# Performance work log

Hardware: AMD Instinct MI355X
Metric: run time of the kernel (lower is better)

Reference implementation:

```python
import jax, jax.numpy as jnp
import numpy as np

NR, NL, K, TOPK, C, B = 4096, 16384, 8, 10, 16, 4
W_OCC, W_MDN, W_INT = 0.2, 1.0, 0.1
LOG2PI = float(np.log(2.0 * np.pi))


def setup_inputs() -> dict:
    key = jax.random.key(0)
    ks = jax.random.split(key, 12)
    radar_indices = jnp.concatenate([
        jax.random.randint(ks[0], (NR, 1), 0, B),
        jax.random.randint(ks[1], (NR, 1), 0, 41),
        jax.random.randint(ks[2], (NR, 2), 0, 176),
    ], axis=1).astype(jnp.int32)
    lidar_indices = jnp.concatenate([
        jax.random.randint(ks[3], (NL, 1), 0, B),
        jax.random.randint(ks[4], (NL, 1), 0, 41),
        jax.random.randint(ks[5], (NL, 2), 0, 176),
    ], axis=1).astype(jnp.int32)
    return {
        'mu_off': jax.random.normal(ks[6], (NR, K, 3)) * 2.0,
        'log_sig_off': jax.random.normal(ks[7], (NR, K, 3)) * 0.3,
        'mu_int': jax.random.normal(ks[8], (NR, K, 1)),
        'occ_logit': jax.random.normal(ks[9], (NR, K, 1)),
        'mix_logit': jax.random.normal(ks[10], (NR, K, 1)),
        'lidar_features': jax.random.normal(ks[11], (NL, C)),
        'radar_indices': radar_indices,
        'lidar_indices': lidar_indices,
        'gt_topk': TOPK,
    }


def _match(radar_indices, lidar_indices, topk):
    # per-batch top-k nearest lidar voxels for each radar voxel (vectorized:
    # dense masked distance matrix replaces the per-batch python loop)
    rb, lb = radar_indices[:, 0], lidar_indices[:, 0]
    rpos = radar_indices[:, 1:].astype(jnp.float32)  # (Nr,3) zyx
    lpos = lidar_indices[:, 1:].astype(jnp.float32)  # (Nl,3)
    d2 = ((rpos * rpos).sum(-1)[:, None] + (lpos * lpos).sum(-1)[None, :]
          - 2.0 * (rpos @ lpos.T))  # (Nr,Nl) squared dist, same order as cdist
    same = rb[:, None] == lb[None, :]
    d2 = jnp.where(same, d2, jnp.inf)  # cross-batch pairs excluded
    _, nn_idx = jax.lax.top_k(-d2, topk)  # (Nr,topk) smallest distances
    matched = same.any(axis=1)  # (Nr,)
    offs_zyx = (lidar_indices[nn_idx, 1:]
                - radar_indices[:, None, 1:]).astype(jnp.float32)  # (Nr,topk,3)
    offs_zyx = jnp.where(matched[:, None, None], offs_zyx, 0.0)
    return matched, nn_idx, offs_zyx


def reference(mu_off, log_sig_off, mu_int, occ_logit, mix_logit,
              lidar_features, radar_indices, lidar_indices, gt_topk):
    matched, nn_idx, offs_zyx = _match(radar_indices, lidar_indices, gt_topk)
    gt_feat = jnp.where(matched[:, None, None], lidar_features[nn_idx], 0.0)  # (Nr,T,C)
    y = offs_zyx[..., ::-1]  # flip zyx -> xyz, (Nr,T,3)

    # occupancy BCE-with-logits against matched mask
    occ_any = occ_logit[..., 0].max(axis=1)  # (Nr,)
    tgt = matched.astype(occ_any.dtype)
    occ_loss = (tgt * jax.nn.softplus(-occ_any)
                + (1.0 - tgt) * jax.nn.softplus(occ_any)).mean()

    # MDN log-prob: (Nr,T,K) mixture components
    log_pi = jax.nn.log_softmax(mix_logit[..., 0], axis=1)  # (Nr,K)
    mu_ = mu_off[:, None, :, :]       # (Nr,1,K,3)
    ls_ = log_sig_off[:, None, :, :]
    sigma2 = jnp.exp(2.0 * ls_) + 1e-12
    y_ = y[:, :, None, :]             # (Nr,T,1,3)
    logN = -0.5 * (((y_ - mu_) ** 2) / sigma2 + 2.0 * ls_ + LOG2PI).sum(-1)  # (Nr,T,K)
    log_post = logN + log_pi[:, None, :]
    logp = jax.nn.logsumexp(log_post, axis=-1)  # (Nr,T)

    # masked means emulate boolean-index-then-mean over matched rows
    m = matched.astype(jnp.float32)
    cnt = m.sum()
    T = logp.shape[1]
    mdn_nll = -(logp * m[:, None]).sum() / (cnt * T)

    # intensity loss (C % 4 == 0 path)
    gt_int = gt_feat.reshape(gt_feat.shape[0], gt_feat.shape[1], C // 4, 4)[..., 3].mean(axis=2)  # (Nr,T)
    r = jax.nn.softmax(log_post, axis=-1)  # (Nr,T,K) responsibilities
    term = r * jnp.abs(mu_int[:, None, :, 0] - gt_int[:, :, None])  # (Nr,T,K)
    int_loss = (term * m[:, None, None]).sum() / (cnt * T * r.shape[-1])

    return W_OCC * occ_loss + W_MDN * mdn_nll + W_INT * int_loss
```

## Files before the change

kernel.cpp:

```cpp
#include <hip/hip_runtime.h>
#include <cstdint>

#define NRAD 4096
#define NLID 16384
#define KMIX 8
#define TOPK 10
#define CF   16
#define LOG2PI 1.8378770664093453f

static constexpr unsigned INF_D2 = 62851u;

__device__ __forceinline__ void insert_key(unsigned (&t)[TOPK], unsigned key) {
#pragma unroll
    for (int i = TOPK - 1; i >= 1; --i) {
        unsigned hi = key > t[i - 1] ? key : t[i - 1];
        t[i] = hi < t[i] ? hi : t[i];
    }
    t[0] = key < t[0] ? key : t[0];
}

__device__ __forceinline__ void merge10(unsigned (&t)[TOPK], int lane,
                                        unsigned& mine, unsigned& first, unsigned& tenth) {
#pragma unroll
    for (int r = 0; r < TOPK; ++r) {
        unsigned v = t[0];
#pragma unroll
        for (int off = 32; off >= 1; off >>= 1) {
            unsigned o = __shfl_xor(v, off, 64);
            v = o < v ? o : v;
        }
        if (t[0] == v) {
#pragma unroll
            for (int i = 0; i < TOPK - 1; ++i) t[i] = t[i + 1];
            t[TOPK - 1] = 0xFFFFFFFFu;
        }
        if (lane == r) mine = v;
        if (r == 0) first = v;
        if (r == TOPK - 1) tenth = v;
    }
}

__device__ __forceinline__ float waveReduceSum(float v) {
#pragma unroll
    for (int off = 32; off >= 1; off >>= 1) v += __shfl_down(v, off, 64);
    return v;
}

__global__ __launch_bounds__(1024) void prep_kernel(
        const int* __restrict__ lidar_indices,
        const int* __restrict__ radar_indices,
        unsigned* __restrict__ packed_full,
        uint2* __restrict__ compacted,
        int* __restrict__ rbin,
        int* __restrict__ ctrl) {
    __shared__ int lcur, rcur;
    int tid = threadIdx.x, lane = tid & 63, myb = blockIdx.x;
    if (tid == 0) { lcur = 0; rcur = 0; }
    __syncthreads();

#pragma unroll
    for (int it = 0; it < NLID / 1024; ++it) {
        int i = it * 1024 + tid;
        int4 li = ((const int4*)lidar_indices)[i];
        unsigned pos = ((unsigned)li.y << 16) | ((unsigned)li.z << 8) | (unsigned)li.w;
        bool mine = (li.x == myb);
        if (mine) packed_full[i] = ((unsigned)li.x << 22) | pos;
        unsigned long long mask = __ballot(mine);
        if (mine) {
            int leader = __ffsll(mask) - 1;
            int off = (int)__popcll(mask & ((1ull << lane) - 1ull));
            int s = 0;
            if (lane == leader) s = atomicAdd(&lcur, (int)__popcll(mask));
            s = __shfl(s, leader, 64);
            compacted[myb * NLID + s + off] = make_uint2(pos, (unsigned)i);
        }
    }

#pragma unroll
    for (int it = 0; it < NRAD / 1024; ++it) {
        int r = it * 1024 + tid;
        int rb = radar_indices[r * 4];
        bool mine = (rb == myb);
        unsigned long long mask = __ballot(mine);
        if (mine) {
            int leader = __ffsll(mask) - 1;
            int off = (int)__popcll(mask & ((1ull << lane) - 1ull));
            int s = 0;
            if (lane == leader) s = atomicAdd(&rcur, (int)__popcll(mask));
            s = __shfl(s, leader, 64);
            rbin[myb * NRAD + s + off] = r;
        }
    }

    __syncthreads();
    if (tid == 0) { ctrl[myb] = lcur; ctrl[12 + myb] = rcur; }
    if (myb == 0 && tid >= 64 && tid < 69) ctrl[4 + (tid - 64)] = 0;
}

__global__ __launch_bounds__(256) void topk_kernel(
        const uint2* __restrict__ compacted,
        const unsigned* __restrict__ packed_full,
        const int* __restrict__ ctrl,
        const int* __restrict__ rbin,
        const int* __restrict__ radar_indices,
        int* __restrict__ nn_out, int* __restrict__ matched_out) {
    int lane = threadIdx.x & 63;
    int g = blockIdx.x * 4 + (threadIdx.x >> 6);
    int r0 = ctrl[12], r1 = ctrl[13], r2 = ctrl[14];
    int cum1 = r0, cum2 = r0 + r1, cum3 = cum2 + r2;
    int gb = (g >= cum1) + (g >= cum2) + (g >= cum3);
    int gbase = gb == 0 ? 0 : (gb == 1 ? cum1 : (gb == 2 ? cum2 : cum3));
    int row = rbin[gb * NRAD + (g - gbase)];

    int4 ri = ((const int4*)radar_indices)[row];
    int rb = ri.x, rz = ri.y, ry = ri.z, rx = ri.w;
    int c_cnt = ctrl[rb];

    unsigned t[TOPK];
#pragma unroll
    for (int i = 0; i < TOPK; ++i) t[i] = 0xFFFFFFFFu;

    const uint4* src = (const uint4*)(compacted + rb * NLID);
    int iters = (c_cnt + 127) >> 7;
    uint4 q = src[lane];
    for (int it = 0; it < iters; ++it) {
        uint4 qn = q;
        if (it + 1 < iters) qn = src[(it + 1) * 64 + lane];
        int c0 = (it * 64 + lane) * 2;
        {
            int dz = (int)((q.x >> 16) & 63u)  - rz;
            int dy = (int)((q.x >> 8)  & 255u) - ry;
            int dx = (int)(q.x & 255u)         - rx;
            unsigned d2 = (unsigned)(__mul24(dz, dz) + __mul24(dy, dy) + __mul24(dx, dx));
            unsigned key = (c0 < c_cnt) ? ((d2 << 14) | q.y) : 0xFFFFFFFFu;
            if (key < t[TOPK - 1]) insert_key(t, key);
        }
        {
            int dz = (int)((q.z >> 16) & 63u)  - rz;
            int dy = (int)((q.z >> 8)  & 255u) - ry;
            int dx = (int)(q.z & 255u)         - rx;
            unsigned d2 = (unsigned)(__mul24(dz, dz) + __mul24(dy, dy) + __mul24(dx, dx));
            unsigned key = (c0 + 1 < c_cnt) ? ((d2 << 14) | q.w) : 0xFFFFFFFFu;
            if (key < t[TOPK - 1]) insert_key(t, key);
        }
        q = qn;
    }

    unsigned mine = 0, first = 0, tenth = 0;
    merge10(t, lane, mine, first, tenth);
    bool matched = true;

    if (tenth == 0xFFFFFFFFu) {
#pragma unroll
        for (int i = 0; i < TOPK; ++i) t[i] = 0xFFFFFFFFu;
        for (int it = 0; it < NLID / 256; ++it) {
            uint4 p4 = ((const uint4*)packed_full)[it * 64 + lane];
            unsigned base = it * 256 + lane * 4;
            unsigned ps[4] = {p4.x, p4.y, p4.z, p4.w};
#pragma unroll
            for (int j = 0; j < 4; ++j) {
                unsigned p = ps[j];
                int b  = (int)(p >> 22);
                int dz = (int)((p >> 16) & 63u)  - rz;
                int dy = (int)((p >> 8)  & 255u) - ry;
                int dx = (int)(p & 255u)         - rx;
                unsigned d2 = (unsigned)(__mul24(dz, dz) + __mul24(dy, dy) + __mul24(dx, dx));
                unsigned hi = (b == rb) ? d2 : INF_D2;
                insert_key(t, (hi << 14) | (base + j));
            }
        }
        merge10(t, lane, mine, first, tenth);
        matched = first < (INF_D2 << 14);
    }

    if (lane < TOPK) nn_out[row * TOPK + lane] = (int)(mine & 0x3FFFu);
    if (lane == 0)   matched_out[row] = matched ? 1 : 0;
}

__global__ __launch_bounds__(256) void mdn_kernel(
        const float* __restrict__ mu_off, const float* __restrict__ log_sig_off,
        const float* __restrict__ mu_int, const float* __restrict__ occ_logit,
        const float* __restrict__ mix_logit, const float* __restrict__ lidar_features,
        const int* __restrict__ radar_indices, const int* __restrict__ lidar_indices,
        const int* __restrict__ nn, const int* __restrict__ matched,
        float* __restrict__ accum,
        unsigned* __restrict__ dctr,
        float* __restrict__ out) {
    int gid = blockIdx.x * 256 + threadIdx.x;
    int n  = gid / TOPK;
    int tt = gid - n * TOPK;
    int m  = matched[n];
    float mf = (float)m;
    int nni = nn[gid];

    int4 ri = ((const int4*)radar_indices)[n];
    int4 li = ((const int4*)lidar_indices)[nni];
    float y0 = mf * (float)(li.w - ri.w);
    float y1 = mf * (float)(li.z - ri.z);
    float y2 = mf * (float)(li.y - ri.y);

    float mix[KMIX];
    float mmax = -1e30f;
#pragma unroll
    for (int k = 0; k < KMIX; ++k) {
        mix[k] = mix_logit[n * KMIX + k];
        mmax = fmaxf(mmax, mix[k]);
    }
    float msum = 0.f;
#pragma unroll
    for (int k = 0; k < KMIX; ++k) msum += expf(mix[k] - mmax);
    float logZ = mmax + logf(msum);

    float lpost[KMIX];
    float pmax = -1e30f;
#pragma unroll
    for (int k = 0; k < KMIX; ++k) {
        int bidx = (n * KMIX + k) * 3;
        float mu0 = mu_off[bidx + 0], mu1 = mu_off[bidx + 1], mu2 = mu_off[bidx + 2];
        float l0 = log_sig_off[bidx + 0], l1 = log_sig_off[bidx + 1], l2 = log_sig_off[bidx + 2];
        float s0 = expf(2.f * l0) + 1e-12f;
        float s1 = expf(2.f * l1) + 1e-12f;
        float s2 = expf(2.f * l2) + 1e-12f;
        float d0 = y0 - mu0, d1 = y1 - mu1, d2v = y2 - mu2;
        float q = d0 * d0 / s0 + d1 * d1 / s1 + d2v * d2v / s2
                + 2.f * (l0 + l1 + l2) + 3.f * LOG2PI;
        lpost[k] = -0.5f * q + (mix[k] - logZ);
        pmax = fmaxf(pmax, lpost[k]);
    }
    float ex[KMIX];
    float se = 0.f;
#pragma unroll
    for (int k = 0; k < KMIX; ++k) { ex[k] = expf(lpost[k] - pmax); se += ex[k]; }
    float logp = pmax + logf(se);

    float gt = 0.f;
    if (m) {
        const float* lf = lidar_features + nni * CF;
        gt = 0.25f * (lf[3] + lf[7] + lf[11] + lf[15]);
    }
    float inv_se = 1.f / se;
    float isum = 0.f;
#pragma unroll
    for (int k = 0; k < KMIX; ++k)
        isum += ex[k] * inv_se * fabsf(mu_int[n * KMIX + k] - gt);

    float lp = mf * logp;
    float ip = mf * isum;
    float oc = 0.f, mc = 0.f;
    if (tt == 0) {
        float oa = -1e30f;
#pragma unroll
        for (int k = 0; k < KMIX; ++k) oa = fmaxf(oa, occ_logit[n * KMIX + k]);
        float soft_abs = log1pf(expf(-fabsf(oa)));
        oc = mf * (soft_abs + fmaxf(-oa, 0.f)) + (1.f - mf) * (soft_abs + fmaxf(oa, 0.f));
        mc = mf;
    }

    lp = waveReduceSum(lp); ip = waveReduceSum(ip);
    oc = waveReduceSum(oc); mc = waveReduceSum(mc);
    __shared__ float sA[4], sB[4], sC[4], sD[4];
    int wid = threadIdx.x >> 6, lane = threadIdx.x & 63;
    if (lane == 0) { sA[wid] = lp; sB[wid] = ip; sC[wid] = oc; sD[wid] = mc; }
    __syncthreads();
    if (threadIdx.x == 0) {
        atomicAdd(&accum[0], sA[0] + sA[1] + sA[2] + sA[3]);
        atomicAdd(&accum[1], sB[0] + sB[1] + sB[2] + sB[3]);
        atomicAdd(&accum[2], sC[0] + sC[1] + sC[2] + sC[3]);
        atomicAdd(&accum[3], sD[0] + sD[1] + sD[2] + sD[3]);
        __threadfence();
        unsigned done = atomicAdd(dctr, 1u);
        if (done == gridDim.x - 1) {
            __threadfence();
            float a = __hip_atomic_load(&accum[0], __ATOMIC_RELAXED, __HIP_MEMORY_SCOPE_AGENT);
            float b = __hip_atomic_load(&accum[1], __ATOMIC_RELAXED, __HIP_MEMORY_SCOPE_AGENT);
            float c = __hip_atomic_load(&accum[2], __ATOMIC_RELAXED, __HIP_MEMORY_SCOPE_AGENT);
            float d = __hip_atomic_load(&accum[3], __ATOMIC_RELAXED, __HIP_MEMORY_SCOPE_AGENT);
            float occ_loss = c / (float)NRAD;
            float mdn_nll  = -a / (d * (float)TOPK);
            float int_loss = b / (d * (float)TOPK * (float)KMIX);
            out[0] = 0.2f * occ_loss + mdn_nll + 0.1f * int_loss;
        }
    }
}

extern "C" void kernel_launch(void* const* d_in, const int* in_sizes, int n_in,
                              void* d_out, int out_size, void* d_ws, size_t ws_size,
                              hipStream_t stream) {
    const float* mu_off         = (const float*)d_in[0];
    const float* log_sig_off    = (const float*)d_in[1];
    const float* mu_int         = (const float*)d_in[2];
    const float* occ_logit      = (const float*)d_in[3];
    const float* mix_logit      = (const float*)d_in[4];
    const float* lidar_features = (const float*)d_in[5];
    const int*   radar_indices  = (const int*)d_in[6];
    const int*   lidar_indices  = (const int*)d_in[7];
    float* out = (float*)d_out;

    char* ws = (char*)d_ws;
    unsigned* packed_full = (unsigned*)(ws + 0);
    uint2*    compacted   = (uint2*)(ws + 65536);
    int*      ctrl        = (int*)(ws + 589824);
    int*      nn          = (int*)(ws + 589888);
    int*      matched     = (int*)(ws + 753728);
    int*      rbin        = (int*)(ws + 770112);

    float*    accum = (float*)(ctrl + 4);
    unsigned* dctr  = (unsigned*)(ctrl + 8);

    hipLaunchKernelGGL(prep_kernel, dim3(4), dim3(1024), 0, stream,
                       lidar_indices, radar_indices, packed_full, compacted, rbin, ctrl);
    hipLaunchKernelGGL(topk_kernel, dim3(NRAD / 4), dim3(256), 0, stream,
                       compacted, packed_full, ctrl, rbin, radar_indices, nn, matched);
    hipLaunchKernelGGL(mdn_kernel, dim3(NRAD * TOPK / 256), dim3(256), 0, stream,
                       mu_off, log_sig_off, mu_int, occ_logit, mix_logit,
                       lidar_features, radar_indices, lidar_indices,
                       nn, matched, accum, dctr, out);
}
```

Before: 121.3 us.

## Fuse top-k matching with MDN loss and preload indices in prep kernel

Folds the MDN/intensity/occupancy loss computation into the top-k kernel. Each wave now uses its merged top-k result directly, with lanes below TOPK taking one neighbor each, so the nn/matched global arrays and a third kernel launch go away. The prep kernel also issues all lidar and radar index loads up front into registers so the loads overlap before the ballot/compaction loops. The cost is more register pressure in the fused kernel and only 10 of 64 lanes doing MDN work per wave, and the completion counter now covers 1024 blocks instead of 160.

```diff
diff --git a/kernel.cpp b/kernel.cpp
--- a/kernel.cpp
+++ b/kernel.cpp
@@ -56,15 +56,24 @@
     __shared__ int lcur, rcur;
     int tid = threadIdx.x, lane = tid & 63, myb = blockIdx.x;
     if (tid == 0) { lcur = 0; rcur = 0; }
+
+    int4 li[NLID / 1024];
+#pragma unroll
+    for (int it = 0; it < NLID / 1024; ++it)
+        li[it] = ((const int4*)lidar_indices)[it * 1024 + tid];
+    int rb4[NRAD / 1024];
+#pragma unroll
+    for (int it = 0; it < NRAD / 1024; ++it)
+        rb4[it] = ((const int4*)radar_indices)[it * 1024 + tid].x;
+
     __syncthreads();
 
 #pragma unroll
     for (int it = 0; it < NLID / 1024; ++it) {
         int i = it * 1024 + tid;
-        int4 li = ((const int4*)lidar_indices)[i];
-        unsigned pos = ((unsigned)li.y << 16) | ((unsigned)li.z << 8) | (unsigned)li.w;
-        bool mine = (li.x == myb);
-        if (mine) packed_full[i] = ((unsigned)li.x << 22) | pos;
+        unsigned pos = ((unsigned)li[it].y << 16) | ((unsigned)li[it].z << 8) | (unsigned)li[it].w;
+        bool mine = (li[it].x == myb);
+        if (mine) packed_full[i] = ((unsigned)li[it].x << 22) | pos;
         unsigned long long mask = __ballot(mine);
         if (mine) {
             int leader = __ffsll(mask) - 1;
@@ -79,8 +88,7 @@
 #pragma unroll
     for (int it = 0; it < NRAD / 1024; ++it) {
         int r = it * 1024 + tid;
-        int rb = radar_indices[r * 4];
-        bool mine = (rb == myb);
+        bool mine = (rb4[it] == myb);
         unsigned long long mask = __ballot(mine);
         if (mine) {
             int leader = __ffsll(mask) - 1;
@@ -97,13 +105,19 @@
     if (myb == 0 && tid >= 64 && tid < 69) ctrl[4 + (tid - 64)] = 0;
 }
 
-__global__ __launch_bounds__(256) void topk_kernel(
+__global__ __launch_bounds__(256) void topk_mdn_kernel(
         const uint2* __restrict__ compacted,
         const unsigned* __restrict__ packed_full,
-        const int* __restrict__ ctrl,
+        int* __restrict__ ctrl,
         const int* __restrict__ rbin,
         const int* __restrict__ radar_indices,
-        int* __restrict__ nn_out, int* __restrict__ matched_out) {
+        const int* __restrict__ lidar_indices,
+        const float* __restrict__ mu_off, const float* __restrict__ log_sig_off,
+        const float* __restrict__ mu_int, const float* __restrict__ occ_logit,
+        const float* __restrict__ mix_logit, const float* __restrict__ lidar_features,
+        float* __restrict__ out) {
+    float* accum = (float*)(ctrl + 4);
+    unsigned* dctr = (unsigned*)(ctrl + 8);
     int lane = threadIdx.x & 63;
     int g = blockIdx.x * 4 + (threadIdx.x >> 6);
     int r0 = ctrl[12], r1 = ctrl[13], r2 = ctrl[14];
@@ -173,31 +187,13 @@
         matched = first < (INF_D2 << 14);
     }
 
-    if (lane < TOPK) nn_out[row * TOPK + lane] = (int)(mine & 0x3FFFu);
-    if (lane == 0)   matched_out[row] = matched ? 1 : 0;
-}
-
-__global__ __launch_bounds__(256) void mdn_kernel(
-        const float* __restrict__ mu_off, const float* __restrict__ log_sig_off,
-        const float* __restrict__ mu_int, const float* __restrict__ occ_logit,
-        const float* __restrict__ mix_logit, const float* __restrict__ lidar_features,
-        const int* __restrict__ radar_indices, const int* __restrict__ lidar_indices,
-        const int* __restrict__ nn, const int* __restrict__ matched,
-        float* __restrict__ accum,
-        unsigned* __restrict__ dctr,
-        float* __restrict__ out) {
-    int gid = blockIdx.x * 256 + threadIdx.x;
-    int n  = gid / TOPK;
-    int tt = gid - n * TOPK;
-    int m  = matched[n];
-    float mf = (float)m;
-    int nni = nn[gid];
-
-    int4 ri = ((const int4*)radar_indices)[n];
+    int n = row;
+    float mf = matched ? 1.f : 0.f;
+    int nni = (int)(mine & 0x3FFFu);
     int4 li = ((const int4*)lidar_indices)[nni];
-    float y0 = mf * (float)(li.w - ri.w);
-    float y1 = mf * (float)(li.z - ri.z);
-    float y2 = mf * (float)(li.y - ri.y);
+    float y0 = mf * (float)(li.w - rx);
+    float y1 = mf * (float)(li.z - ry);
+    float y2 = mf * (float)(li.y - rz);
 
     float mix[KMIX];
     float mmax = -1e30f;
@@ -222,9 +218,9 @@
         float s1 = expf(2.f * l1) + 1e-12f;
         float s2 = expf(2.f * l2) + 1e-12f;
         float d0 = y0 - mu0, d1 = y1 - mu1, d2v = y2 - mu2;
-        float q = d0 * d0 / s0 + d1 * d1 / s1 + d2v * d2v / s2
-                + 2.f * (l0 + l1 + l2) + 3.f * LOG2PI;
-        lpost[k] = -0.5f * q + (mix[k] - logZ);
+        float qv = d0 * d0 / s0 + d1 * d1 / s1 + d2v * d2v / s2
+                 + 2.f * (l0 + l1 + l2) + 3.f * LOG2PI;
+        lpost[k] = -0.5f * qv + (mix[k] - logZ);
         pmax = fmaxf(pmax, lpost[k]);
     }
     float ex[KMIX];
@@ -234,7 +230,7 @@
     float logp = pmax + logf(se);
 
     float gt = 0.f;
-    if (m) {
+    if (matched) {
         const float* lf = lidar_features + nni * CF;
         gt = 0.25f * (lf[3] + lf[7] + lf[11] + lf[15]);
     }
@@ -244,10 +240,10 @@
     for (int k = 0; k < KMIX; ++k)
         isum += ex[k] * inv_se * fabsf(mu_int[n * KMIX + k] - gt);
 
-    float lp = mf * logp;
-    float ip = mf * isum;
+    float lp = (lane < TOPK) ? mf * logp : 0.f;
+    float ip = (lane < TOPK) ? mf * isum : 0.f;
     float oc = 0.f, mc = 0.f;
-    if (tt == 0) {
+    if (lane == 0) {
         float oa = -1e30f;
 #pragma unroll
         for (int k = 0; k < KMIX; ++k) oa = fmaxf(oa, occ_logit[n * KMIX + k]);
@@ -259,7 +255,7 @@
     lp = waveReduceSum(lp); ip = waveReduceSum(ip);
     oc = waveReduceSum(oc); mc = waveReduceSum(mc);
     __shared__ float sA[4], sB[4], sC[4], sD[4];
-    int wid = threadIdx.x >> 6, lane = threadIdx.x & 63;
+    int wid = threadIdx.x >> 6;
     if (lane == 0) { sA[wid] = lp; sB[wid] = ip; sC[wid] = oc; sD[wid] = mc; }
     __syncthreads();
     if (threadIdx.x == 0) {
@@ -300,19 +296,12 @@
     unsigned* packed_full = (unsigned*)(ws + 0);
     uint2*    compacted   = (uint2*)(ws + 65536);
     int*      ctrl        = (int*)(ws + 589824);
-    int*      nn          = (int*)(ws + 589888);
-    int*      matched     = (int*)(ws + 753728);
-    int*      rbin        = (int*)(ws + 770112);
-
-    float*    accum = (float*)(ctrl + 4);
-    unsigned* dctr  = (unsigned*)(ctrl + 8);
+    int*      rbin        = (int*)(ws + 589888);
 
     hipLaunchKernelGGL(prep_kernel, dim3(4), dim3(1024), 0, stream,
                        lidar_indices, radar_indices, packed_full, compacted, rbin, ctrl);
-    hipLaunchKernelGGL(topk_kernel, dim3(NRAD / 4), dim3(256), 0, stream,
-                       compacted, packed_full, ctrl, rbin, radar_indices, nn, matched);
-    hipLaunchKernelGGL(mdn_kernel, dim3(NRAD * TOPK / 256), dim3(256), 0, stream,
+    hipLaunchKernelGGL(topk_mdn_kernel, dim3(NRAD / 4), dim3(256), 0, stream,
+                       compacted, packed_full, ctrl, rbin, radar_indices, lidar_indices,
                        mu_off, log_sig_off, mu_int, occ_logit, mix_logit,
-                       lidar_features, radar_indices, lidar_indices,
-                       nn, matched, accum, dctr, out);
-}
+                       lidar_features, out);
+}
```

Measured after the change: 162.6 us. 34.0% more time.

## Bin lidar points by y coordinate and prune top-k search to nearby bins

Applied to the files above, without the earlier changes.

The prep kernel now counting-sorts each batch's lidar points into 176 bins keyed on the y coordinate and writes per-bin offsets. The top-k kernel first scans only bins within ±16 of the radar row's y and falls back to a full scan of the batch when the tenth-best distance cannot be proven below the window boundary. This is meant to cut the per-wave brute-force scan of roughly 4096 candidates down to a narrow slab. In exchange it drops the radar grouping by batch, which may lower cache locality, and the scan loop no longer double-buffers its loads. Atomic bin scatter also makes the order of points within a bin nondeterministic, so ties are broken by the stored index key.

```diff
diff --git a/kernel.cpp b/kernel.cpp
--- a/kernel.cpp
+++ b/kernel.cpp
@@ -6,6 +6,7 @@
 #define KMIX 8
 #define TOPK 10
 #define CF   16
+#define NBIN 176
 #define LOG2PI 1.8378770664093453f
 
 static constexpr unsigned INF_D2 = 62851u;
@@ -46,54 +47,65 @@
     return v;
 }
 
+__device__ __forceinline__ void scan_range(unsigned (&t)[TOPK], const uint2* __restrict__ base,
+                                           int s, int e, int rz, int ry, int rx, int lane) {
+    for (int i = s + lane; i < e; i += 64) {
+        uint2 c = base[i];
+        int dz = (int)((c.x >> 16) & 63u)  - rz;
+        int dy = (int)((c.x >> 8)  & 255u) - ry;
+        int dx = (int)(c.x & 255u)         - rx;
+        unsigned d2 = (unsigned)(__mul24(dz, dz) + __mul24(dy, dy) + __mul24(dx, dx));
+        unsigned key = (d2 << 14) | c.y;
+        if (key < t[TOPK - 1]) insert_key(t, key);
+    }
+}
+
 __global__ __launch_bounds__(1024) void prep_kernel(
         const int* __restrict__ lidar_indices,
-        const int* __restrict__ radar_indices,
         unsigned* __restrict__ packed_full,
         uint2* __restrict__ compacted,
-        int* __restrict__ rbin,
+        int* __restrict__ binoff_g,
         int* __restrict__ ctrl) {
-    __shared__ int lcur, rcur;
-    int tid = threadIdx.x, lane = tid & 63, myb = blockIdx.x;
-    if (tid == 0) { lcur = 0; rcur = 0; }
+    __shared__ int hist[NBIN];
+    __shared__ int binoff_s[NBIN + 1];
+    __shared__ int bcur[NBIN];
+    int tid = threadIdx.x, myb = blockIdx.x;
+    if (tid < NBIN) hist[tid] = 0;
+
+    int4 li[NLID / 1024];
+#pragma unroll
+    for (int it = 0; it < NLID / 1024; ++it)
+        li[it] = ((const int4*)lidar_indices)[it * 1024 + tid];
+    __syncthreads();
+
+#pragma unroll
+    for (int it = 0; it < NLID / 1024; ++it)
+        if (li[it].x == myb) atomicAdd(&hist[li[it].z], 1);
+    __syncthreads();
+
+    if (tid <= NBIN) {
+        int s = 0;
+        for (int j = 0; j < tid; ++j) s += hist[j];
+        binoff_s[tid] = s;
+    }
+    __syncthreads();
+    if (tid < NBIN) bcur[tid] = binoff_s[tid];
     __syncthreads();
 
 #pragma unroll
     for (int it = 0; it < NLID / 1024; ++it) {
         int i = it * 1024 + tid;
-        int4 li = ((const int4*)lidar_indices)[i];
-        unsigned pos = ((unsigned)li.y << 16) | ((unsigned)li.z << 8) | (unsigned)li.w;
-        bool mine = (li.x == myb);
-        if (mine) packed_full[i] = ((unsigned)li.x << 22) | pos;
-        unsigned long long mask = __ballot(mine);
-        if (mine) {
-            int leader = __ffsll(mask) - 1;
-            int off = (int)__popcll(mask & ((1ull << lane) - 1ull));
-            int s = 0;
-            if (lane == leader) s = atomicAdd(&lcur, (int)__popcll(mask));
-            s = __shfl(s, leader, 64);
-            compacted[myb * NLID + s + off] = make_uint2(pos, (unsigned)i);
-        }
-    }
-
-#pragma unroll
-    for (int it = 0; it < NRAD / 1024; ++it) {
-        int r = it * 1024 + tid;
-        int rb = radar_indices[r * 4];
-        bool mine = (rb == myb);
-        unsigned long long mask = __ballot(mine);
-        if (mine) {
-            int leader = __ffsll(mask) - 1;
-            int off = (int)__popcll(mask & ((1ull << lane) - 1ull));
-            int s = 0;
-            if (lane == leader) s = atomicAdd(&rcur, (int)__popcll(mask));
-            s = __shfl(s, leader, 64);
-            rbin[myb * NRAD + s + off] = r;
-        }
-    }
-
-    __syncthreads();
-    if (tid == 0) { ctrl[myb] = lcur; ctrl[12 + myb] = rcur; }
+        unsigned pos = ((unsigned)li[it].y << 16) | ((unsigned)li[it].z << 8) | (unsigned)li[it].w;
+        if (li[it].x == myb) {
+            packed_full[i] = ((unsigned)li[it].x << 22) | pos;
+            int dst = atomicAdd(&bcur[li[it].z], 1);
+            compacted[myb * NLID + dst] = make_uint2(pos, (unsigned)i);
+        }
+    }
+
+    __syncthreads();
+    if (tid <= NBIN) binoff_g[myb * (NBIN + 1) + tid] = binoff_s[tid];
+    if (tid == 0)    ctrl[myb] = binoff_s[NBIN];
     if (myb == 0 && tid >= 64 && tid < 69) ctrl[4 + (tid - 64)] = 0;
 }
 
@@ -101,61 +113,49 @@
         const uint2* __restrict__ compacted,
         const unsigned* __restrict__ packed_full,
         const int* __restrict__ ctrl,
-        const int* __restrict__ rbin,
+        const int* __restrict__ binoff_g,
         const int* __restrict__ radar_indices,
         int* __restrict__ nn_out, int* __restrict__ matched_out) {
     int lane = threadIdx.x & 63;
-    int g = blockIdx.x * 4 + (threadIdx.x >> 6);
-    int r0 = ctrl[12], r1 = ctrl[13], r2 = ctrl[14];
-    int cum1 = r0, cum2 = r0 + r1, cum3 = cum2 + r2;
-    int gb = (g >= cum1) + (g >= cum2) + (g >= cum3);
-    int gbase = gb == 0 ? 0 : (gb == 1 ? cum1 : (gb == 2 ? cum2 : cum3));
-    int row = rbin[gb * NRAD + (g - gbase)];
-
+    int row  = blockIdx.x * 4 + (threadIdx.x >> 6);
     int4 ri = ((const int4*)radar_indices)[row];
     int rb = ri.x, rz = ri.y, ry = ri.z, rx = ri.w;
-    int c_cnt = ctrl[rb];
+    const int* boff = binoff_g + rb * (NBIN + 1);
+
+    int lo = ry - 16; lo = lo < 0 ? 0 : lo;
+    int hi = ry + 17; hi = hi > NBIN ? NBIN : hi;
+    int s = boff[lo], e = boff[hi];
 
     unsigned t[TOPK];
 #pragma unroll
     for (int i = 0; i < TOPK; ++i) t[i] = 0xFFFFFFFFu;
 
-    const uint4* src = (const uint4*)(compacted + rb * NLID);
-    int iters = (c_cnt + 127) >> 7;
-    uint4 q = src[lane];
-    for (int it = 0; it < iters; ++it) {
-        uint4 qn = q;
-        if (it + 1 < iters) qn = src[(it + 1) * 64 + lane];
-        int c0 = (it * 64 + lane) * 2;
-        {
-            int dz = (int)((q.x >> 16) & 63u)  - rz;
-            int dy = (int)((q.x >> 8)  & 255u) - ry;
-            int dx = (int)(q.x & 255u)         - rx;
-            unsigned d2 = (unsigned)(__mul24(dz, dz) + __mul24(dy, dy) + __mul24(dx, dx));
-            unsigned key = (c0 < c_cnt) ? ((d2 << 14) | q.y) : 0xFFFFFFFFu;
-            if (key < t[TOPK - 1]) insert_key(t, key);
-        }
-        {
-            int dz = (int)((q.z >> 16) & 63u)  - rz;
-            int dy = (int)((q.z >> 8)  & 255u) - ry;
-            int dx = (int)(q.z & 255u)         - rx;
-            unsigned d2 = (unsigned)(__mul24(dz, dz) + __mul24(dy, dy) + __mul24(dx, dx));
-            unsigned key = (c0 + 1 < c_cnt) ? ((d2 << 14) | q.w) : 0xFFFFFFFFu;
-            if (key < t[TOPK - 1]) insert_key(t, key);
-        }
-        q = qn;
-    }
-
-    unsigned mine = 0, first = 0, tenth = 0;
+    const uint2* base = compacted + rb * NLID;
+    scan_range(t, base, s, e, rz, ry, rx, lane);
+
+    unsigned mine = 0xFFFFFFFFu, first = 0, tenth = 0;
     merge10(t, lane, mine, first, tenth);
     bool matched = true;
+
+    unsigned lim = 0xFFFFFFFFu;
+    if (lo > 0)    { unsigned d = (unsigned)(ry - lo + 1); unsigned v = d * d; lim = v < lim ? v : lim; }
+    if (hi < NBIN) { unsigned d = (unsigned)(hi - ry);     unsigned v = d * d; lim = v < lim ? v : lim; }
+
+    if ((tenth >> 14) >= lim) {
+#pragma unroll
+        for (int i = 0; i < TOPK; ++i) t[i] = 0xFFFFFFFFu;
+        t[0] = mine;
+        scan_range(t, base, boff[0], s, rz, ry, rx, lane);
+        scan_range(t, base, e, boff[NBIN], rz, ry, rx, lane);
+        merge10(t, lane, mine, first, tenth);
+    }
 
     if (tenth == 0xFFFFFFFFu) {
 #pragma unroll
         for (int i = 0; i < TOPK; ++i) t[i] = 0xFFFFFFFFu;
         for (int it = 0; it < NLID / 256; ++it) {
             uint4 p4 = ((const uint4*)packed_full)[it * 64 + lane];
-            unsigned base = it * 256 + lane * 4;
+            unsigned bse = it * 256 + lane * 4;
             unsigned ps[4] = {p4.x, p4.y, p4.z, p4.w};
 #pragma unroll
             for (int j = 0; j < 4; ++j) {
@@ -165,8 +165,8 @@
                 int dy = (int)((p >> 8)  & 255u) - ry;
                 int dx = (int)(p & 255u)         - rx;
                 unsigned d2 = (unsigned)(__mul24(dz, dz) + __mul24(dy, dy) + __mul24(dx, dx));
-                unsigned hi = (b == rb) ? d2 : INF_D2;
-                insert_key(t, (hi << 14) | (base + j));
+                unsigned hi2 = (b == rb) ? d2 : INF_D2;
+                insert_key(t, (hi2 << 14) | (bse + j));
             }
         }
         merge10(t, lane, mine, first, tenth);
@@ -302,15 +302,15 @@
     int*      ctrl        = (int*)(ws + 589824);
     int*      nn          = (int*)(ws + 589888);
     int*      matched     = (int*)(ws + 753728);
-    int*      rbin        = (int*)(ws + 770112);
+    int*      binoff_g    = (int*)(ws + 770112);
 
     float*    accum = (float*)(ctrl + 4);
     unsigned* dctr  = (unsigned*)(ctrl + 8);
 
     hipLaunchKernelGGL(prep_kernel, dim3(4), dim3(1024), 0, stream,
-                       lidar_indices, radar_indices, packed_full, compacted, rbin, ctrl);
+                       lidar_indices, packed_full, compacted, binoff_g, ctrl);
     hipLaunchKernelGGL(topk_kernel, dim3(NRAD / 4), dim3(256), 0, stream,
-                       compacted, packed_full, ctrl, rbin, radar_indices, nn, matched);
+                       compacted, packed_full, ctrl, binoff_g, radar_indices, nn, matched);
     hipLaunchKernelGGL(mdn_kernel, dim3(NRAD * TOPK / 256), dim3(256), 0, stream,
                        mu_off, log_sig_off, mu_int, occ_logit, mix_logit,
                        lidar_features, radar_indices, lidar_indices,
```

Result: faster. 112.5 us (-7.2%).
